# Kernel tuning notes

Hardware: AMD Instinct MI355X
Metric: run time of the kernel (lower is better)

## Reference

```python
import jax, jax.numpy as jnp
import numpy as np

K = 5            # carafe kernel size
CK = 3           # content conv kernel size = max(3, K-2)
EMB = 64         # embedding size
FILTERS = 128    # output filters


def conv1x1(x, w, b=None):
    y = jnp.einsum('bhwc,co->bhwo', x, w)
    return y if b is None else y + b


def conv_same(x, w, b):
    y = jax.lax.conv_general_dilated(x, w, (1, 1), 'SAME',
                                     dimension_numbers=('NHWC', 'HWIO', 'NHWC'))
    return y + b


def up2(x):
    return jnp.repeat(jnp.repeat(x, 2, axis=1), 2, axis=2)


def setup_inputs() -> dict:
    key = jax.random.key(0)
    ks = jax.random.split(key, 12)
    B, H, W, Cf = 2, 128, 128, 128
    h, w, Cc = 64, 64, 128
    s = 0.05
    return {
        'fine': jax.random.normal(ks[0], (B, H, W, Cf), jnp.float32),
        'coarse': jax.random.normal(ks[1], (B, h, w, Cc), jnp.float32),
        # gate 1x1 conv (Cc -> 1)
        'w_gate': jax.random.normal(ks[2], (Cc, 1), jnp.float32) * s,
        'b_gate': jnp.zeros((1,), jnp.float32),
        # SemiShift: fine 1x1 (no bias), coarse 1x1 (bias), shared content conv (EMB -> K*K)
        'w_sfine': jax.random.normal(ks[3], (Cf, EMB), jnp.float32) * s,
        'w_scoarse': jax.random.normal(ks[4], (Cc, EMB), jnp.float32) * s,
        'b_scoarse': jnp.zeros((EMB,), jnp.float32),
        'w_content': jax.random.normal(ks[5], (CK, CK, EMB, K * K), jnp.float32) * s,
        'b_content': jnp.zeros((K * K,), jnp.float32),
        # output 1x1 convs
        'w_coarse': jax.random.normal(ks[6], (Cc, FILTERS), jnp.float32) * s,
        'b_coarse': jnp.zeros((FILTERS,), jnp.float32),
        'w_fineout': jax.random.normal(ks[7], (FILTERS, FILTERS), jnp.float32) * s,
        'b_fineout': jnp.zeros((FILTERS,), jnp.float32),
    }


def reference(fine, coarse, w_gate, b_gate, w_sfine, w_scoarse, b_scoarse,
              w_content, b_content, w_coarse, b_coarse, w_fineout, b_fineout):
    B, h, w, Cc = coarse.shape
    H, W = fine.shape[1], fine.shape[2]

    # gate branch
    gate = jax.nn.sigmoid(conv1x1(coarse, w_gate, b_gate))
    gate = up2(gate)  # [B,H,W,1]

    # SemiShift kernel prediction
    f = conv1x1(fine, w_sfine)                     # no bias
    f = conv_same(f, w_content, b_content)         # [B,H,W,K*K]
    c = conv1x1(coarse, w_scoarse, b_scoarse)
    c = conv_same(c, w_content, b_content)         # [B,h,w,K*K]
    kernel = jax.nn.softmax(f + up2(c), axis=-1)   # [B,H,W,K*K]

    # CarafeConvolution: extract_patches (TF layout: [pos, ch] innermost) + NN up + grouped matmul
    p = K // 2
    xp = jnp.pad(coarse, ((0, 0), (p, p), (p, p), (0, 0)))
    patches = jnp.stack([xp[:, r:r + h, cc:cc + w, :]
                         for r in range(K) for cc in range(K)], axis=3)  # [B,h,w,K*K,Cc]
    patches = patches.reshape(B, h, w, K * K * Cc)
    patches = up2(patches)                          # [B,H,W,K*K*Cc]
    # faithful reshape as in source (group_size=1): (B,H,W,Cc,K*K)
    feat = patches.reshape(B, H, W, Cc, K * K)
    carafe = jnp.einsum('bhwck,bhwk->bhwc', feat, kernel)  # [B,H,W,Cc]

    coarse_out = conv1x1(carafe, w_coarse, b_coarse)        # [B,H,W,FILTERS]
    fine_out = conv1x1(coarse_out, w_fineout, b_fineout)    # note: applied to coarse_out as in source
    return gate * fine_out + (1.0 - gate) * coarse_out
```

## Files before the change

### kernel.cpp

```cpp
#include <hip/hip_runtime.h>
#include <hip/hip_bf16.h>
#include <cstdint>
#include <cstddef>

#define KSZ 5
#define KK 25
#define EMB 64
#define CC 128
#define FILTERS 128

typedef __attribute__((ext_vector_type(8))) short short8;
typedef __attribute__((ext_vector_type(4))) float floatx4;

__device__ inline unsigned short f32_to_bf16(float f) {
    union { float f; unsigned u; } v; v.f = f;
    unsigned u = v.u;
    unsigned r = u + 0x7FFF + ((u >> 16) & 1);
    return (unsigned short)(r >> 16);
}

__global__ void wtrans_all_kernel(const float* __restrict__ w_sfine,
                                  const float* __restrict__ w_scoarse,
                                  const float* __restrict__ w_content,
                                  const float* __restrict__ w_coarse,
                                  const float* __restrict__ w_fineout,
                                  unsigned short* __restrict__ wsfT,
                                  unsigned short* __restrict__ wscT,
                                  unsigned short* __restrict__ wconT,
                                  unsigned short* __restrict__ wcT,
                                  unsigned short* __restrict__ wfT) {
    int i = blockIdx.x * blockDim.x + threadIdx.x;
    if (i < 8192) {
        int n = i >> 7, k = i & 127;
        wsfT[i] = f32_to_bf16(w_sfine[k * 64 + n]);
    } else if (i < 16384) {
        int j = i - 8192;
        int n = j >> 7, k = j & 127;
        wscT[j] = f32_to_bf16(w_scoarse[k * 64 + n]);
    } else if (i < 34816) {
        int j = i - 16384;
        int n = j / 576, k = j - n * 576;
        float v = (n < 25) ? w_content[k * 25 + n] : 0.0f;
        wconT[j] = f32_to_bf16(v);
    } else if (i < 51200) {
        int j = i - 34816;
        int o = j >> 7, k = j & 127;
        wcT[j] = f32_to_bf16(w_coarse[k * 128 + o]);
    } else if (i < 67584) {
        int j = i - 51200;
        int o = j >> 7, k = j & 127;
        wfT[j] = f32_to_bf16(w_fineout[k * 128 + o]);
    }
}

#define XS_P 136
__global__ __launch_bounds__(256) void embed_both_kernel(
        const float* __restrict__ xf, const unsigned short* __restrict__ wTf,
        const float* __restrict__ xc, const unsigned short* __restrict__ wTc,
        const float* __restrict__ bias_c,
        unsigned short* __restrict__ yf, unsigned short* __restrict__ yc,
        int nf) {
    __shared__ unsigned short Xs[128 * XS_P];
    __shared__ unsigned short Ws[64 * XS_P];
    int tid = threadIdx.x;
    bool is_f = (int)blockIdx.x < nf;
    int blk = is_f ? blockIdx.x : (blockIdx.x - nf);
    const float* x = is_f ? xf : xc;
    const unsigned short* wT = is_f ? wTf : wTc;
    const float* bias = is_f ? nullptr : bias_c;
    unsigned short* y = is_f ? yf : yc;
    size_t row0 = (size_t)blk * 128;

    {
        const float4* src = (const float4*)(x + row0 * 128);
        for (int ci = tid; ci < 4096; ci += 256) {
            int r = ci >> 5, c4 = ci & 31;
            float4 v = src[ci];
            uint2 u;
            u.x = (unsigned)f32_to_bf16(v.x) | ((unsigned)f32_to_bf16(v.y) << 16);
            u.y = (unsigned)f32_to_bf16(v.z) | ((unsigned)f32_to_bf16(v.w) << 16);
            *(uint2*)(&Xs[r * XS_P + c4 * 4]) = u;
        }
        const uint4* wsrc = (const uint4*)wT;
        for (int ci = tid; ci < 1024; ci += 256) {
            int n = ci >> 4, k8 = ci & 15;
            *(uint4*)(&Ws[n * XS_P + k8 * 8]) = wsrc[ci];
        }
    }
    __syncthreads();

    int wid = tid >> 6, lane = tid & 63;
    int lr = lane & 15, hi = lane >> 4, lk = hi * 8;

    floatx4 acc[2][4];
    #pragma unroll
    for (int mi = 0; mi < 2; ++mi)
        #pragma unroll
        for (int ni = 0; ni < 4; ++ni)
            acc[mi][ni] = (floatx4){0.f, 0.f, 0.f, 0.f};

    #pragma unroll
    for (int kk = 0; kk < 128; kk += 32) {
        short8 a[2], bb[4];
        #pragma unroll
        for (int mi = 0; mi < 2; ++mi)
            a[mi] = *(const short8*)(&Xs[(wid * 32 + mi * 16 + lr) * XS_P + kk + lk]);
        #pragma unroll
        for (int ni = 0; ni < 4; ++ni)
            bb[ni] = *(const short8*)(&Ws[(ni * 16 + lr) * XS_P + kk + lk]);
        #pragma unroll
        for (int mi = 0; mi < 2; ++mi)
            #pragma unroll
            for (int ni = 0; ni < 4; ++ni)
                acc[mi][ni] = __builtin_amdgcn_mfma_f32_16x16x32_bf16(a[mi], bb[ni], acc[mi][ni], 0, 0, 0);
    }

    #pragma unroll
    for (int mi = 0; mi < 2; ++mi) {
        #pragma unroll
        for (int ni = 0; ni < 4; ++ni) {
            int col = ni * 16 + lr;
            float bs = bias ? bias[col] : 0.0f;
            #pragma unroll
            for (int j = 0; j < 4; ++j) {
                int row = wid * 32 + mi * 16 + hi * 4 + j;
                y[(row0 + row) * EMB + col] = f32_to_bf16(acc[mi][ni][j] + bs);
            }
        }
    }
}

#define SP 72
#define SB 584
__global__ __launch_bounds__(256) void content_both_kernel(
        const unsigned short* __restrict__ embf,
        const unsigned short* __restrict__ embc,
        const unsigned short* __restrict__ wT,
        const float* __restrict__ bias,
        float* __restrict__ yf, float* __restrict__ yc,
        int nf) {
    __shared__ unsigned short Es[6 * 34 * SP];
    __shared__ unsigned short Bs[32 * SB];
    int tid = threadIdx.x;
    bool is_f = (int)blockIdx.x < nf;
    int blk = is_f ? blockIdx.x : (blockIdx.x - nf);
    const unsigned short* emb = is_f ? embf : embc;
    float* y = is_f ? yf : yc;
    int HT = is_f ? 32 : 16;
    int WT = is_f ? 4 : 2;
    int Hh = is_f ? 128 : 64;
    int Ww = is_f ? 128 : 64;

    int bx = blk % WT;
    int t = blk / WT;
    int by = t % HT;
    int b = t / HT;

    for (int ci = tid; ci < 1632; ci += 256) {
        int pi = ci >> 3, e8 = ci & 7;
        int hy = pi / 34, hx = pi - hy * 34;
        int gy = by * 4 + hy - 1, gx = bx * 32 + hx - 1;
        uint4 v = {0u, 0u, 0u, 0u};
        if (gy >= 0 && gy < Hh && gx >= 0 && gx < Ww)
            v = *(const uint4*)(emb + (((size_t)(b * Hh + gy)) * Ww + gx) * EMB + e8 * 8);
        *(uint4*)(&Es[pi * SP + e8 * 8]) = v;
    }
    for (int ci = tid; ci < 2304; ci += 256) {
        int n = ci / 72, k8 = ci - n * 72;
        *(uint4*)(&Bs[n * SB + k8 * 8]) = *(const uint4*)(wT + n * 576 + k8 * 8);
    }
    __syncthreads();

    int wid = tid >> 6, lane = tid & 63;
    int lr = lane & 15, hi = lane >> 4, lk = hi * 8;

    floatx4 acc[2][2];
    #pragma unroll
    for (int mi = 0; mi < 2; ++mi)
        #pragma unroll
        for (int ni = 0; ni < 2; ++ni)
            acc[mi][ni] = (floatx4){0.f, 0.f, 0.f, 0.f};

    #pragma unroll
    for (int tap = 0; tap < 9; ++tap) {
        int dy = tap / 3, dx = tap - dy * 3;
        #pragma unroll
        for (int ks = 0; ks < 2; ++ks) {
            short8 a[2], bb[2];
            #pragma unroll
            for (int mi = 0; mi < 2; ++mi) {
                int p = wid * 32 + mi * 16 + lr;
                int r = p >> 5, c = p & 31;
                a[mi] = *(const short8*)(&Es[((r + dy) * 34 + (c + dx)) * SP + ks * 32 + lk]);
            }
            #pragma unroll
            for (int ni = 0; ni < 2; ++ni)
                bb[ni] = *(const short8*)(&Bs[(ni * 16 + lr) * SB + tap * 64 + ks * 32 + lk]);
            #pragma unroll
            for (int mi = 0; mi < 2; ++mi)
                #pragma unroll
                for (int ni = 0; ni < 2; ++ni)
                    acc[mi][ni] = __builtin_amdgcn_mfma_f32_16x16x32_bf16(a[mi], bb[ni], acc[mi][ni], 0, 0, 0);
        }
    }

    #pragma unroll
    for (int mi = 0; mi < 2; ++mi) {
        #pragma unroll
        for (int ni = 0; ni < 2; ++ni) {
            int n = ni * 16 + lr;
            if (n < KK) {
                float bs = bias[n];
                #pragma unroll
                for (int j = 0; j < 4; ++j) {
                    int p = wid * 32 + mi * 16 + hi * 4 + j;
                    int r = p >> 5, c = p & 31;
                    size_t gq = ((size_t)(b * Hh + by * 4 + r)) * Ww + bx * 32 + c;
                    y[gq * KK + n] = acc[mi][ni][j] + bs;
                }
            }
        }
    }
}

__global__ __launch_bounds__(256) void carafe_gate_kernel(
        const float* __restrict__ coarse,
        const float* __restrict__ f_conv,
        const float* __restrict__ c_conv,
        const float* __restrict__ w_gate,
        const float* __restrict__ b_gate,
        unsigned short* __restrict__ xout,
        float* __restrict__ g_gate,
        int h, int w) {
    __shared__ float patch[KK * CC];
    __shared__ float wsm[4 * 32];
    int cpix = blockIdx.x;
    int npix = h * w;
    int b = cpix / npix;
    int rem = cpix - b * npix;
    int cy = rem / w;
    int cx = rem - cy * w;
    int tid = threadIdx.x;

    for (int ci = tid; ci < 800; ci += 256) {
        int k = ci >> 5;
        int c4 = (ci & 31) << 2;
        int dy = (k * 205) >> 10;
        int dx = k - dy * 5;
        int py = cy + dy - 2, px = cx + dx - 2;
        float4 v = {0.f, 0.f, 0.f, 0.f};
        if (py >= 0 && py < h && px >= 0 && px < w)
            v = *(const float4*)(coarse + (((size_t)(b * h + py)) * w + px) * CC + c4);
        *(float4*)(&patch[ci << 2]) = v;
    }

    int wid = tid >> 6, lane = tid & 63;
    int fy = 2 * cy + (wid >> 1);
    int fx = 2 * cx + (wid & 1);
    int H2 = 2 * h, W2 = 2 * w;
    size_t fq = ((size_t)(b * H2 + fy)) * W2 + fx;
    {
        int k = lane & 31;
        float v = -1e30f;
        if (k < KK)
            v = f_conv[fq * KK + k] + c_conv[(size_t)cpix * KK + k];
        float m = v;
        #pragma unroll
        for (int mask = 16; mask > 0; mask >>= 1)
            m = fmaxf(m, __shfl_xor(m, mask, 32));
        float e = (k < KK) ? __expf(v - m) : 0.0f;
        float s = e;
        #pragma unroll
        for (int mask = 16; mask > 0; mask >>= 1)
            s += __shfl_xor(s, mask, 32);
        if (lane < 32)
            wsm[wid * 32 + k] = e / s;
    }
    __syncthreads();

    if (wid == 0) {
        float acc = patch[12 * CC + lane] * w_gate[lane]
                  + patch[12 * CC + lane + 64] * w_gate[lane + 64];
        #pragma unroll
        for (int off = 32; off > 0; off >>= 1)
            acc += __shfl_down(acc, off, 64);
        if (lane == 0) {
            float z = acc + b_gate[0];
            g_gate[cpix] = 1.0f / (1.0f + __expf(-z));
        }
    }

    float wreg[28];
    #pragma unroll
    for (int j4 = 0; j4 < 7; ++j4)
        *(float4*)(&wreg[j4 * 4]) = *(const float4*)(&wsm[wid * 32 + j4 * 4]);

    unsigned short* outp = xout + fq * CC;
    #pragma unroll
    for (int cp = 0; cp < 2; ++cp) {
        int c = lane + 64 * cp;
        const float* pp = patch + c * KK;
        float acc = 0.0f;
        #pragma unroll
        for (int j = 0; j < KK; ++j)
            acc += wreg[j] * pp[j];
        outp[c] = f32_to_bf16(acc);
    }
}

#define LDSP 136
__global__ __launch_bounds__(256) void final_kernel(
        const unsigned short* __restrict__ X,
        const unsigned short* __restrict__ WcT,
        const unsigned short* __restrict__ WfT,
        const float* __restrict__ b_coarse,
        const float* __restrict__ b_fineout,
        const float* __restrict__ gate,
        float* __restrict__ out) {
    __shared__ unsigned short Xs[64 * LDSP];
    __shared__ unsigned short Ws[128 * LDSP];
    int tid = threadIdx.x;
    int row0 = blockIdx.x * 64;

    {
        const uint4* src = (const uint4*)(X + (size_t)row0 * 128);
        for (int ci = tid; ci < 1024; ci += 256) {
            int r = ci >> 4, c = ci & 15;
            *(uint4*)(&Xs[r * LDSP + c * 8]) = src[ci];
        }
        const uint4* wsrc = (const uint4*)WcT;
        for (int ci = tid; ci < 2048; ci += 256) {
            int r = ci >> 4, c = ci & 15;
            *(uint4*)(&Ws[r * LDSP + c * 8]) = wsrc[ci];
        }
    }
    __syncthreads();

    int wid = tid >> 6, lane = tid & 63;
    int wm = wid >> 1, wn = wid & 1;
    int lr = lane & 15;
    int lk = (lane >> 4) * 8;
    int lrow4 = (lane >> 4) * 4;

    floatx4 acc1[2][4];
    #pragma unroll
    for (int mi = 0; mi < 2; ++mi)
        #pragma unroll
        for (int ni = 0; ni < 4; ++ni)
            acc1[mi][ni] = (floatx4){0.f, 0.f, 0.f, 0.f};

    #pragma unroll
    for (int kk = 0; kk < 128; kk += 32) {
        short8 a[2], bb[4];
        #pragma unroll
        for (int mi = 0; mi < 2; ++mi)
            a[mi] = *(const short8*)(&Xs[(wm * 32 + mi * 16 + lr) * LDSP + kk + lk]);
        #pragma unroll
        for (int ni = 0; ni < 4; ++ni)
            bb[ni] = *(const short8*)(&Ws[(wn * 64 + ni * 16 + lr) * LDSP + kk + lk]);
        #pragma unroll
        for (int mi = 0; mi < 2; ++mi)
            #pragma unroll
            for (int ni = 0; ni < 4; ++ni)
                acc1[mi][ni] = __builtin_amdgcn_mfma_f32_16x16x32_bf16(a[mi], bb[ni], acc1[mi][ni], 0, 0, 0);
    }
    __syncthreads();

    {
        const uint4* wsrc = (const uint4*)WfT;
        for (int ci = tid; ci < 2048; ci += 256) {
            int r = ci >> 4, c = ci & 15;
            *(uint4*)(&Ws[r * LDSP + c * 8]) = wsrc[ci];
        }
    }
    #pragma unroll
    for (int mi = 0; mi < 2; ++mi) {
        #pragma unroll
        for (int ni = 0; ni < 4; ++ni) {
            int col = wn * 64 + ni * 16 + lr;
            float bc = b_coarse[col];
            #pragma unroll
            for (int j = 0; j < 4; ++j) {
                int row = wm * 32 + mi * 16 + lrow4 + j;
                float v = acc1[mi][ni][j] + bc;
                acc1[mi][ni][j] = v;
                Xs[row * LDSP + col] = f32_to_bf16(v);
            }
        }
    }
    __syncthreads();

    floatx4 acc2[2][4];
    #pragma unroll
    for (int mi = 0; mi < 2; ++mi)
        #pragma unroll
        for (int ni = 0; ni < 4; ++ni)
            acc2[mi][ni] = (floatx4){0.f, 0.f, 0.f, 0.f};

    #pragma unroll
    for (int kk = 0; kk < 128; kk += 32) {
        short8 a[2], bb[4];
        #pragma unroll
        for (int mi = 0; mi < 2; ++mi)
            a[mi] = *(const short8*)(&Xs[(wm * 32 + mi * 16 + lr) * LDSP + kk + lk]);
        #pragma unroll
        for (int ni = 0; ni < 4; ++ni)
            bb[ni] = *(const short8*)(&Ws[(wn * 64 + ni * 16 + lr) * LDSP + kk + lk]);
        #pragma unroll
        for (int mi = 0; mi < 2; ++mi)
            #pragma unroll
            for (int ni = 0; ni < 4; ++ni)
                acc2[mi][ni] = __builtin_amdgcn_mfma_f32_16x16x32_bf16(a[mi], bb[ni], acc2[mi][ni], 0, 0, 0);
    }

    #pragma unroll
    for (int mi = 0; mi < 2; ++mi) {
        #pragma unroll
        for (int ni = 0; ni < 4; ++ni) {
            int col = wn * 64 + ni * 16 + lr;
            float bf = b_fineout[col];
            #pragma unroll
            for (int j = 0; j < 4; ++j) {
                int row = wm * 32 + mi * 16 + lrow4 + j;
                int q = row0 + row;
                int b = q >> 14;
                int remq = q & 16383;
                int fy = remq >> 7, fx = remq & 127;
                float g = gate[(b << 12) + ((fy >> 1) << 6) + (fx >> 1)];
                float co = acc1[mi][ni][j];
                float fo = acc2[mi][ni][j] + bf;
                out[(size_t)q * FILTERS + col] = g * fo + (1.0f - g) * co;
            }
        }
    }
}

extern "C" void kernel_launch(void* const* d_in, const int* in_sizes, int n_in,
                              void* d_out, int out_size, void* d_ws, size_t ws_size,
                              hipStream_t stream) {
    const float* fine      = (const float*)d_in[0];
    const float* coarse    = (const float*)d_in[1];
    const float* w_gate    = (const float*)d_in[2];
    const float* b_gate    = (const float*)d_in[3];
    const float* w_sfine   = (const float*)d_in[4];
    const float* w_scoarse = (const float*)d_in[5];
    const float* b_scoarse = (const float*)d_in[6];
    const float* w_content = (const float*)d_in[7];
    const float* b_content = (const float*)d_in[8];
    const float* w_coarse  = (const float*)d_in[9];
    const float* b_coarse  = (const float*)d_in[10];
    const float* w_fineout = (const float*)d_in[11];
    const float* b_fineout = (const float*)d_in[12];
    float* out = (float*)d_out;

    const int B = 2, H = 128, W = 128, h = 64, w = 64;
    const int MF = B * H * W;
    const int MC = B * h * w;

    char* ws = (char*)d_ws;
    size_t off = 0;
    auto alloc = [&](size_t bytes) {
        void* p = ws + off;
        off = (off + bytes + 255) & ~(size_t)255;
        return p;
    };
    float* g_gate            = (float*)alloc((size_t)MC * 4);
    unsigned short* f_emb    = (unsigned short*)alloc((size_t)MF * EMB * 2);
    unsigned short* c_emb    = (unsigned short*)alloc((size_t)MC * EMB * 2);
    float* f_conv            = (float*)alloc((size_t)MF * KK * 4);
    float* c_conv            = (float*)alloc((size_t)MC * KK * 4);
    unsigned short* x_bf16   = (unsigned short*)alloc((size_t)MF * CC * 2);
    unsigned short* wsfT     = (unsigned short*)alloc(64 * 128 * 2);
    unsigned short* wscT     = (unsigned short*)alloc(64 * 128 * 2);
    unsigned short* wconT    = (unsigned short*)alloc(32 * 576 * 2);
    unsigned short* wcT      = (unsigned short*)alloc(128 * 128 * 2);
    unsigned short* wfT      = (unsigned short*)alloc(128 * 128 * 2);

    const int NEF = MF / 128;
    const int NEC = MC / 128;
    const int NCF = B * (H / 4) * (W / 32);
    const int NCC = B * (h / 4) * (w / 32);

    wtrans_all_kernel<<<264, 256, 0, stream>>>(w_sfine, w_scoarse, w_content, w_coarse, w_fineout,
                                               wsfT, wscT, wconT, wcT, wfT);
    embed_both_kernel<<<NEF + NEC, 256, 0, stream>>>(fine, wsfT, coarse, wscT, b_scoarse,
                                                     f_emb, c_emb, NEF);
    content_both_kernel<<<NCF + NCC, 256, 0, stream>>>(f_emb, c_emb, wconT, b_content,
                                                       f_conv, c_conv, NCF);
    carafe_gate_kernel<<<MC, 256, 0, stream>>>(coarse, f_conv, c_conv, w_gate, b_gate,
                                               x_bf16, g_gate, h, w);
    final_kernel<<<MF / 64, 256, 0, stream>>>(x_bf16, wcT, wfT, b_coarse, b_fineout, g_gate, out);
}
```

Measured before the change: 58.03 us.

## Load embed GEMM operands directly from global and prefetch fineout weights into registers

```diff
diff --git a/kernel.cpp b/kernel.cpp
--- a/kernel.cpp
+++ b/kernel.cpp
@@ -53,79 +53,57 @@
     }
 }
 
-#define XS_P 136
 __global__ __launch_bounds__(256) void embed_both_kernel(
         const float* __restrict__ xf, const unsigned short* __restrict__ wTf,
         const float* __restrict__ xc, const unsigned short* __restrict__ wTc,
         const float* __restrict__ bias_c,
         unsigned short* __restrict__ yf, unsigned short* __restrict__ yc,
         int nf) {
-    __shared__ unsigned short Xs[128 * XS_P];
-    __shared__ unsigned short Ws[64 * XS_P];
-    int tid = threadIdx.x;
     bool is_f = (int)blockIdx.x < nf;
     int blk = is_f ? blockIdx.x : (blockIdx.x - nf);
     const float* x = is_f ? xf : xc;
     const unsigned short* wT = is_f ? wTf : wTc;
     const float* bias = is_f ? nullptr : bias_c;
     unsigned short* y = is_f ? yf : yc;
-    size_t row0 = (size_t)blk * 128;
-
-    {
-        const float4* src = (const float4*)(x + row0 * 128);
-        for (int ci = tid; ci < 4096; ci += 256) {
-            int r = ci >> 5, c4 = ci & 31;
-            float4 v = src[ci];
-            uint2 u;
-            u.x = (unsigned)f32_to_bf16(v.x) | ((unsigned)f32_to_bf16(v.y) << 16);
-            u.y = (unsigned)f32_to_bf16(v.z) | ((unsigned)f32_to_bf16(v.w) << 16);
-            *(uint2*)(&Xs[r * XS_P + c4 * 4]) = u;
-        }
-        const uint4* wsrc = (const uint4*)wT;
-        for (int ci = tid; ci < 1024; ci += 256) {
-            int n = ci >> 4, k8 = ci & 15;
-            *(uint4*)(&Ws[n * XS_P + k8 * 8]) = wsrc[ci];
-        }
-    }
-    __syncthreads();
-
+
+    int tid = threadIdx.x;
     int wid = tid >> 6, lane = tid & 63;
     int lr = lane & 15, hi = lane >> 4, lk = hi * 8;
 
-    floatx4 acc[2][4];
-    #pragma unroll
-    for (int mi = 0; mi < 2; ++mi)
-        #pragma unroll
-        for (int ni = 0; ni < 4; ++ni)
-            acc[mi][ni] = (floatx4){0.f, 0.f, 0.f, 0.f};
-
-    #pragma unroll
-    for (int kk = 0; kk < 128; kk += 32) {
-        short8 a[2], bb[4];
-        #pragma unroll
-        for (int mi = 0; mi < 2; ++mi)
-            a[mi] = *(const short8*)(&Xs[(wid * 32 + mi * 16 + lr) * XS_P + kk + lk]);
-        #pragma unroll
-        for (int ni = 0; ni < 4; ++ni)
-            bb[ni] = *(const short8*)(&Ws[(ni * 16 + lr) * XS_P + kk + lk]);
-        #pragma unroll
-        for (int mi = 0; mi < 2; ++mi)
-            #pragma unroll
-            for (int ni = 0; ni < 4; ++ni)
-                acc[mi][ni] = __builtin_amdgcn_mfma_f32_16x16x32_bf16(a[mi], bb[ni], acc[mi][ni], 0, 0, 0);
-    }
-
-    #pragma unroll
-    for (int mi = 0; mi < 2; ++mi) {
+    size_t row0 = (size_t)blk * 64;
+    int arow = wid * 16 + lr;
+    const float* xr = x + (row0 + arow) * 128;
+
+    floatx4 acc[4];
+    #pragma unroll
+    for (int ni = 0; ni < 4; ++ni)
+        acc[ni] = (floatx4){0.f, 0.f, 0.f, 0.f};
+
+    #pragma unroll
+    for (int kk = 0; kk < 4; ++kk) {
+        float4 a0 = *(const float4*)(xr + kk * 32 + lk);
+        float4 a1 = *(const float4*)(xr + kk * 32 + lk + 4);
+        unsigned short ah[8];
+        ah[0] = f32_to_bf16(a0.x); ah[1] = f32_to_bf16(a0.y);
+        ah[2] = f32_to_bf16(a0.z); ah[3] = f32_to_bf16(a0.w);
+        ah[4] = f32_to_bf16(a1.x); ah[5] = f32_to_bf16(a1.y);
+        ah[6] = f32_to_bf16(a1.z); ah[7] = f32_to_bf16(a1.w);
+        short8 a = *(const short8*)ah;
         #pragma unroll
         for (int ni = 0; ni < 4; ++ni) {
-            int col = ni * 16 + lr;
-            float bs = bias ? bias[col] : 0.0f;
-            #pragma unroll
-            for (int j = 0; j < 4; ++j) {
-                int row = wid * 32 + mi * 16 + hi * 4 + j;
-                y[(row0 + row) * EMB + col] = f32_to_bf16(acc[mi][ni][j] + bs);
-            }
+            short8 bb = *(const short8*)(wT + (size_t)(ni * 16 + lr) * 128 + kk * 32 + lk);
+            acc[ni] = __builtin_amdgcn_mfma_f32_16x16x32_bf16(a, bb, acc[ni], 0, 0, 0);
+        }
+    }
+
+    #pragma unroll
+    for (int ni = 0; ni < 4; ++ni) {
+        int col = ni * 16 + lr;
+        float bs = bias ? bias[col] : 0.0f;
+        #pragma unroll
+        for (int j = 0; j < 4; ++j) {
+            int row = wid * 16 + hi * 4 + j;
+            y[(row0 + row) * EMB + col] = f32_to_bf16(acc[ni][j] + bs);
         }
     }
 }
@@ -322,6 +300,13 @@
     int tid = threadIdx.x;
     int row0 = blockIdx.x * 64;
 
+    uint4 wfreg[8];
+    {
+        const uint4* wfsrc = (const uint4*)WfT;
+        #pragma unroll
+        for (int t = 0; t < 8; ++t)
+            wfreg[t] = wfsrc[tid + t * 256];
+    }
     {
         const uint4* src = (const uint4*)(X + (size_t)row0 * 128);
         for (int ci = tid; ci < 1024; ci += 256) {
@@ -367,10 +352,11 @@
     __syncthreads();
 
     {
-        const uint4* wsrc = (const uint4*)WfT;
-        for (int ci = tid; ci < 2048; ci += 256) {
+        #pragma unroll
+        for (int t = 0; t < 8; ++t) {
+            int ci = tid + t * 256;
             int r = ci >> 4, c = ci & 15;
-            *(uint4*)(&Ws[r * LDSP + c * 8]) = wsrc[ci];
+            *(uint4*)(&Ws[r * LDSP + c * 8]) = wfreg[t];
         }
     }
     #pragma unroll
@@ -476,8 +462,8 @@
     unsigned short* wcT      = (unsigned short*)alloc(128 * 128 * 2);
     unsigned short* wfT      = (unsigned short*)alloc(128 * 128 * 2);
 
-    const int NEF = MF / 128;
-    const int NEC = MC / 128;
+    const int NEF = MF / 64;
+    const int NEC = MC / 64;
     const int NCF = B * (H / 4) * (W / 32);
     const int NCC = B * (h / 4) * (w / 32);
 
```

After: 64.96 us. +11.9%, slower.
